# Optimization experiments

Measured on AMD Instinct MI355X. Metric: run time of the kernel, lower is better.

The kernel has to match this reference:

```python
import jax, jax.numpy as jnp
import numpy as np

N = 10000          # nodes
E = 320000         # edges (~32 neighbors/node)
HID = 128          # hidden_channels
NF = 128           # num_filters
NG = 50            # num_gaussians
NB = 6             # num_interactions
CUT = 10.0         # cutoff


def ssp(x):
    # ShiftedSoftplus: softplus(x) - log(2)
    return jax.nn.softplus(x) - jnp.log(2.0).astype(x.dtype)


def setup_inputs() -> dict:
    key = jax.random.key(0)
    ks = jax.random.split(key, 16)
    z = jax.random.randint(ks[0], (N,), 0, 100)
    pos = jax.random.uniform(ks[1], (N, 3), dtype=jnp.float32) * 5.0  # box so d < cutoff
    row = jax.random.randint(ks[2], (E,), 0, N)
    off = jax.random.randint(ks[3], (E,), 1, N)  # avoid self-loops (radius_graph excludes them)
    col = (row + off) % N
    edge_index = jnp.stack([row, col], axis=0)
    nrm = lambda k, s: 0.1 * jax.random.normal(k, s, dtype=jnp.float32)
    return {
        "z": z,
        "pos": pos,
        "edge_index": edge_index,
        "emb": nrm(ks[4], (100, HID)),
        "mlp_w1": nrm(ks[5], (NB, NG, NF)),
        "mlp_b1": jnp.zeros((NB, NF), jnp.float32),
        "mlp_w2": nrm(ks[6], (NB, NF, NF)),
        "mlp_b2": jnp.zeros((NB, NF), jnp.float32),
        "cl1_w": nrm(ks[7], (NB, HID, NF)),
        "cl2_w": nrm(ks[8], (NB, NF, HID)),
        "cl2_b": jnp.zeros((NB, HID), jnp.float32),
        "lin_w": nrm(ks[9], (NB, HID, HID)),
        "lin_b": jnp.zeros((NB, HID), jnp.float32),
        "out_w1": nrm(ks[10], (HID, HID // 2)),
        "out_b1": jnp.zeros((HID // 2,), jnp.float32),
        "out_w2": nrm(ks[11], (HID // 2, 1)),
        "out_b2": jnp.zeros((1,), jnp.float32),
    }


def schnet_fwd(z, pos, edge_index, emb, mlp_w1, mlp_b1, mlp_w2, mlp_b2,
               cl1_w, cl2_w, cl2_b, lin_w, lin_b, out_w1, out_b1, out_w2, out_b2):
    row, col = edge_index[0], edge_index[1]  # j (source), i (target)
    d = jnp.linalg.norm(pos[row] - pos[col], axis=-1)  # [E]
    offsets = jnp.linspace(0.0, CUT, NG)
    coeff = -0.5 / (offsets[1] - offsets[0]) ** 2
    edge_attr = jnp.exp(coeff * (d[:, None] - offsets) ** 2)  # [E, NG]
    C = 0.5 * (jnp.cos(d * jnp.pi / CUT) + 1.0)  # cosine cutoff [E]
    h = emb[z]  # [N, HID]
    n = h.shape[0]
    for k in range(NB):
        # per-edge filter MLP
        W = ssp(edge_attr @ mlp_w1[k] + mlp_b1[k]) @ mlp_w2[k] + mlp_b2[k]
        W = W * C[:, None]  # [E, NF]
        x = h @ cl1_w[k]  # lin1 (no bias) [N, NF]
        msg = x[row] * W  # gather + modulate
        agg = jax.ops.segment_sum(msg, col, num_segments=n)  # scatter-add to targets
        x = agg @ cl2_w[k] + cl2_b[k]  # lin2 [N, HID]
        x = ssp(x)
        x = x @ lin_w[k] + lin_b[k]  # InteractionBlock.lin
        h = h + x  # residual
    h = ssp(h @ out_w1 + out_b1)
    return h @ out_w2 + out_b2  # [N, 1]


def reference(z, pos, edge_index, emb, mlp_w1, mlp_b1, mlp_w2, mlp_b2,
              cl1_w, cl2_w, cl2_b, lin_w, lin_b, out_w1, out_b1, out_w2, out_b2):
    return schnet_fwd(z, pos, edge_index, emb, mlp_w1, mlp_b1, mlp_w2, mlp_b2,
                      cl1_w, cl2_w, cl2_b, lin_w, lin_b, out_w1, out_b1, out_w2, out_b2)
```

## Files before the change

kernel.cpp:

```cpp
#include <hip/hip_runtime.h>
#include <math.h>

#define N_NODES 10000
#define N_EDGES 320000
#define HID 128
#define NF 128
#define NG 50
#define NB 6
#define SCAN_CH 40
#define WFRAG_PER_K 24576
#define NWF_PER_MAT 32768
#define TBL_M 2048
#define DMAX 8.6602540378f

typedef __attribute__((ext_vector_type(8))) short bf16x8;
typedef __attribute__((ext_vector_type(4))) float f32x4;
typedef __attribute__((ext_vector_type(4))) unsigned int u32x4;

__device__ __forceinline__ int pi_map(int f) {
  return (f & ~31) | ((f & 15) << 1) | ((f >> 4) & 1);
}
__device__ __forceinline__ int pinv_map(int g) {
  return (g & ~31) | ((g & 1) << 4) | ((g & 31) >> 1);
}

__device__ __forceinline__ unsigned short f2bf(float f) {
  unsigned u = __float_as_uint(f);
  u += 0x7FFFu + ((u >> 16) & 1u);
  return (unsigned short)(u >> 16);
}
__device__ __forceinline__ float bf2f(unsigned short s) {
  return __uint_as_float(((unsigned)s) << 16);
}
__device__ __forceinline__ unsigned pack2f(float a, float b) {
  return ((__float_as_uint(a) + 0x8000u) >> 16) |
         ((__float_as_uint(b) + 0x8000u) & 0xFFFF0000u);
}
__device__ __forceinline__ float ssp_fast(float x) {
  float t = __expf(-fabsf(x));
  return fmaxf(x, 0.0f) + __logf(1.0f + t) - 0.69314718055994530942f;
}

__global__ __launch_bounds__(256) void k_embed(const int* __restrict__ z,
                                               const float* __restrict__ emb,
                                               float* __restrict__ h) {
  int t = blockIdx.x * 256 + threadIdx.x;
  if (t >= N_NODES * HID) return;
  int i = t >> 7, c = t & 127;
  h[t] = emb[z[i] * HID + c];
}

__global__ __launch_bounds__(256) void k_hist(const int* __restrict__ col,
                                              int* __restrict__ count) {
  int e = blockIdx.x * 256 + threadIdx.x;
  if (e < N_EDGES) atomicAdd(&count[col[e]], 1);
}

__global__ __launch_bounds__(256) void k_scan(const int* __restrict__ count,
                                              int* __restrict__ rowptr,
                                              int* __restrict__ cursor) {
  __shared__ int s_part[256];
  int t = threadIdx.x;
  int begin = t * SCAN_CH, end = min(begin + SCAN_CH, N_NODES);
  int s = 0;
  for (int i = begin; i < end; i++) s += count[i];
  s_part[t] = s;
  __syncthreads();
  for (int off = 1; off < 256; off <<= 1) {
    int v = (t >= off) ? s_part[t - off] : 0;
    __syncthreads();
    s_part[t] += v;
    __syncthreads();
  }
  int run = (t > 0) ? s_part[t - 1] : 0;
  for (int i = begin; i < end; i++) {
    rowptr[i] = run;
    cursor[i] = run;
    run += count[i];
  }
  if (t == 255) rowptr[N_NODES] = N_EDGES;
}

__global__ __launch_bounds__(256) void k_scatter(const int* __restrict__ row,
                                                 const int* __restrict__ col,
                                                 const float* __restrict__ pos,
                                                 int* __restrict__ cursor,
                                                 int2* __restrict__ sorted_ru) {
  int e = blockIdx.x * 256 + threadIdx.x;
  if (e >= N_EDGES) return;
  int c = col[e], r = row[e];
  float dx = pos[3 * r + 0] - pos[3 * c + 0];
  float dy = pos[3 * r + 1] - pos[3 * c + 1];
  float dz = pos[3 * r + 2] - pos[3 * c + 2];
  float d = sqrtf(dx * dx + dy * dy + dz * dz);
  int p = atomicAdd(&cursor[c], 1);
  float u = d * ((float)(TBL_M - 1) / DMAX);
  sorted_ru[p] = make_int2(r, __float_as_int(u));
}

__global__ __launch_bounds__(256) void k_pack(const float* __restrict__ w1,
                                              const float* __restrict__ w2,
                                              unsigned short* __restrict__ wf) {
  const float* w1k = w1 + (size_t)blockIdx.x * NG * NF;
  const float* w2k = w2 + (size_t)blockIdx.x * NF * NF;
  unsigned short* wfk = wf + (size_t)blockIdx.x * WFRAG_PER_K;
  for (int inst = threadIdx.x; inst < 3072; inst += 256) {
    int fi = inst >> 8;
    int wv = (inst >> 6) & 3;
    int lane = inst & 63;
    int r16 = lane & 15, kgrp = lane >> 4;
    bf16x8 v;
#pragma unroll
    for (int j = 0; j < 8; ++j) {
      float val;
      if (fi < 4) {
        int ncol = wv * 32 + r16 + (fi >> 1) * 16;
        int k = (fi & 1) * 32 + kgrp * 8 + j;
        val = (k < NG) ? w1k[k * NF + ncol] : 0.f;
      } else {
        int fi2 = fi - 4;
        int ncol = wv * 32 + r16 + (fi2 >> 2) * 16;
        int kpi = (fi2 & 3) * 32 + kgrp * 8 + j;
        val = w2k[pinv_map(kpi) * NF + ncol];
      }
      v[j] = (short)f2bf(val);
    }
    *(bf16x8*)&wfk[inst * 8] = v;
  }
}

__global__ __launch_bounds__(256) void k_packn(const float* __restrict__ cl1,
                                               const float* __restrict__ cl2,
                                               const float* __restrict__ lin,
                                               unsigned short* __restrict__ nwf) {
  const int mat = blockIdx.x;
  const float* src = (mat < 6) ? cl1 + (size_t)mat * HID * NF
                   : (mat < 12) ? cl2 + (size_t)(mat - 6) * NF * HID
                                : lin + (size_t)(mat - 12) * HID * HID;
  unsigned short* dst = nwf + (size_t)mat * NWF_PER_MAT;
  for (int inst = threadIdx.x; inst < 2048; inst += 256) {
    int fi = inst >> 8;
    int wv = (inst >> 6) & 3;
    int lane = inst & 63;
    int r16 = lane & 15, kgrp = lane >> 4;
    int ncol = wv * 32 + r16 + (fi >> 2) * 16;
    int kb = fi & 3;
    bf16x8 fh, fl;
#pragma unroll
    for (int j = 0; j < 8; ++j) {
      float val = src[(kb * 32 + kgrp * 8 + j) * 128 + ncol];
      unsigned short hh = f2bf(val);
      fh[j] = (short)hh;
      fl[j] = (short)f2bf(val - bf2f(hh));
    }
    *(bf16x8*)&dst[((fi * 4 + wv) * 64 + lane) * 8] = fh;
    *(bf16x8*)&dst[(((fi + 8) * 4 + wv) * 64 + lane) * 8] = fl;
  }
}

__device__ __forceinline__ void stage_hilo(unsigned short* s_hi, unsigned short* s_lo,
                                           int rr, int c4, float4 v) {
  int cs = c4 ^ ((rr & 7) << 3);
  unsigned hax = (__float_as_uint(v.x) + 0x8000u) & 0xFFFF0000u;
  unsigned hay = (__float_as_uint(v.y) + 0x8000u) & 0xFFFF0000u;
  unsigned haz = (__float_as_uint(v.z) + 0x8000u) & 0xFFFF0000u;
  unsigned haw = (__float_as_uint(v.w) + 0x8000u) & 0xFFFF0000u;
  float lx = v.x - __uint_as_float(hax);
  float ly = v.y - __uint_as_float(hay);
  float lz = v.z - __uint_as_float(haz);
  float lw = v.w - __uint_as_float(haw);
  *(uint2*)&s_hi[rr * 128 + cs] = make_uint2((hax >> 16) | hay, (haz >> 16) | haw);
  *(uint2*)&s_lo[rr * 128 + cs] = make_uint2(pack2f(lx, ly), pack2f(lz, lw));
}

__device__ __forceinline__ int swz_idx(int row, int col) {
  return row * 128 + (((col & ~7) ^ ((row & 7) << 3)) | (col & 7));
}

#define KSTEP(accA, accB, kb, BH_A, BL_A, BH_B, BL_B, rowoff)                  \
  {                                                                            \
    bf16x8 ahi = *(const bf16x8*)&s_hi[(rowoff) + (((kb) * 32 + kb0) ^ swz)];  \
    bf16x8 alo = *(const bf16x8*)&s_lo[(rowoff) + (((kb) * 32 + kb0) ^ swz)];  \
    accA = __builtin_amdgcn_mfma_f32_16x16x32_bf16(ahi, BH_A, accA, 0, 0, 0);  \
    accA = __builtin_amdgcn_mfma_f32_16x16x32_bf16(alo, BH_A, accA, 0, 0, 0);  \
    accA = __builtin_amdgcn_mfma_f32_16x16x32_bf16(ahi, BL_A, accA, 0, 0, 0);  \
    accB = __builtin_amdgcn_mfma_f32_16x16x32_bf16(ahi, BH_B, accB, 0, 0, 0);  \
    accB = __builtin_amdgcn_mfma_f32_16x16x32_bf16(alo, BH_B, accB, 0, 0, 0);  \
    accB = __builtin_amdgcn_mfma_f32_16x16x32_bf16(ahi, BL_B, accB, 0, 0, 0);  \
  }
#define MFMA_ALL()                                          \
  {                                                         \
    const int ro0 = r16 * 128;                              \
    KSTEP(a00, a01, 0, bh00, bl00, bh10, bl10, ro0);        \
    KSTEP(a00, a01, 1, bh01, bl01, bh11, bl11, ro0);        \
    KSTEP(a00, a01, 2, bh02, bl02, bh12, bl12, ro0);        \
    KSTEP(a00, a01, 3, bh03, bl03, bh13, bl13, ro0);        \
    const int ro1 = (16 + r16) * 128;                       \
    KSTEP(a10, a11, 0, bh00, bl00, bh10, bl10, ro1);        \
    KSTEP(a10, a11, 1, bh01, bl01, bh11, bl11, ro1);        \
    KSTEP(a10, a11, 2, bh02, bl02, bh12, bl12, ro1);        \
    KSTEP(a10, a11, 3, bh03, bl03, bh13, bl13, ro1);        \
  }
#define LOAD_FRAGS(wfp)                                                              \
  const bf16x8* np = (const bf16x8*)(wfp);                                           \
  const bf16x8 bh00 = np[(0 * 4 + wvid) * 64 + lane], bh01 = np[(1 * 4 + wvid) * 64 + lane], \
               bh02 = np[(2 * 4 + wvid) * 64 + lane], bh03 = np[(3 * 4 + wvid) * 64 + lane], \
               bh10 = np[(4 * 4 + wvid) * 64 + lane], bh11 = np[(5 * 4 + wvid) * 64 + lane], \
               bh12 = np[(6 * 4 + wvid) * 64 + lane], bh13 = np[(7 * 4 + wvid) * 64 + lane], \
               bl00 = np[(8 * 4 + wvid) * 64 + lane], bl01 = np[(9 * 4 + wvid) * 64 + lane], \
               bl02 = np[(10 * 4 + wvid) * 64 + lane], bl03 = np[(11 * 4 + wvid) * 64 + lane], \
               bl10 = np[(12 * 4 + wvid) * 64 + lane], bl11 = np[(13 * 4 + wvid) * 64 + lane], \
               bl12 = np[(14 * 4 + wvid) * 64 + lane], bl13 = np[(15 * 4 + wvid) * 64 + lane];

__global__ __launch_bounds__(256) void k_ngemm(const float* __restrict__ in,
                                               const unsigned short* __restrict__ wf,
                                               float* __restrict__ out,
                                               int nrows) {
  __shared__ __align__(16) float s_buf[32 * 128];
  unsigned short* s_hi = (unsigned short*)s_buf;
  unsigned short* s_lo = s_hi + 32 * 128;
  float* s_out = s_buf;

  const int tid = threadIdx.x;
  const int lane = tid & 63;
  const int wvid = tid >> 6;
  const int r16 = lane & 15;
  const int kgrp = lane >> 4;
  const int kb0 = kgrp * 8;
  const int nc0 = wvid * 32 + r16;
  const int nc1 = nc0 + 16;
  const int r0 = blockIdx.x * 32;

#pragma unroll
  for (int j = 0; j < 4; ++j) {
    int idx4 = j * 256 + tid;
    int rr = idx4 >> 5;
    int c4 = (idx4 & 31) << 2;
    float4 v = make_float4(0.f, 0.f, 0.f, 0.f);
    if (r0 + rr < nrows) v = *(const float4*)&in[(size_t)(r0 + rr) * 128 + c4];
    stage_hilo(s_hi, s_lo, rr, c4, v);
  }
  LOAD_FRAGS(wf);
  __syncthreads();

  f32x4 a00 = {0.f, 0.f, 0.f, 0.f}, a01 = a00, a10 = a00, a11 = a00;
  const int swz = (r16 & 7) << 3;
  MFMA_ALL();
  __syncthreads();

#pragma unroll
  for (int r = 0; r < 4; ++r) {
    int er0 = kgrp * 4 + r, er1 = 16 + kgrp * 4 + r;
    s_out[er0 * 128 + (nc0 ^ ((er0 & 7) << 2))] = a00[r];
    s_out[er0 * 128 + (nc1 ^ ((er0 & 7) << 2))] = a01[r];
    s_out[er1 * 128 + (nc0 ^ ((er1 & 7) << 2))] = a10[r];
    s_out[er1 * 128 + (nc1 ^ ((er1 & 7) << 2))] = a11[r];
  }
  __syncthreads();

#pragma unroll
  for (int j = 0; j < 4; ++j) {
    int idx4 = j * 256 + tid;
    int rr = idx4 >> 5;
    int c4 = (idx4 & 31) << 2;
    if (r0 + rr >= nrows) continue;
    int cs = c4 ^ ((rr & 7) << 2);
    *(float4*)&out[(size_t)(r0 + rr) * 128 + c4] = *(float4*)&s_out[rr * 128 + cs];
  }
}

__global__ __launch_bounds__(256) void k_ngemm2(const float* __restrict__ agg,
                                                const unsigned short* __restrict__ wf_cl2,
                                                const float* __restrict__ b_cl2,
                                                const unsigned short* __restrict__ wf_lin,
                                                const float* __restrict__ b_lin,
                                                float* __restrict__ h,
                                                int nrows) {
  __shared__ __align__(16) float s_buf[32 * 128];
  unsigned short* s_hi = (unsigned short*)s_buf;
  unsigned short* s_lo = s_hi + 32 * 128;
  float* s_out = s_buf;

  const int tid = threadIdx.x;
  const int lane = tid & 63;
  const int wvid = tid >> 6;
  const int r16 = lane & 15;
  const int kgrp = lane >> 4;
  const int kb0 = kgrp * 8;
  const int nc0 = wvid * 32 + r16;
  const int nc1 = nc0 + 16;
  const int r0 = blockIdx.x * 32;
  const int swz = (r16 & 7) << 3;

#pragma unroll
  for (int j = 0; j < 4; ++j) {
    int idx4 = j * 256 + tid;
    int rr = idx4 >> 5;
    int c4 = (idx4 & 31) << 2;
    float4 v = make_float4(0.f, 0.f, 0.f, 0.f);
    if (r0 + rr < nrows) v = *(const float4*)&agg[(size_t)(r0 + rr) * 128 + c4];
    stage_hilo(s_hi, s_lo, rr, c4, v);
  }
  const float bc0 = b_cl2[nc0], bc1 = b_cl2[nc1];
  const float bl0_ = b_lin[nc0], bl1_ = b_lin[nc1];
  __syncthreads();

  f32x4 a00 = {0.f, 0.f, 0.f, 0.f}, a01 = a00, a10 = a00, a11 = a00;
  {
    LOAD_FRAGS(wf_cl2);
    MFMA_ALL();
  }
  __syncthreads();

#pragma unroll
  for (int r = 0; r < 4; ++r) {
    int er0 = kgrp * 4 + r, er1 = 16 + kgrp * 4 + r;
    float t00 = ssp_fast(a00[r] + bc0);
    float t01 = ssp_fast(a01[r] + bc1);
    float t10 = ssp_fast(a10[r] + bc0);
    float t11 = ssp_fast(a11[r] + bc1);
    unsigned u;
    u = (__float_as_uint(t00) + 0x8000u) & 0xFFFF0000u;
    s_hi[swz_idx(er0, nc0)] = (unsigned short)(u >> 16);
    s_lo[swz_idx(er0, nc0)] = (unsigned short)(pack2f(t00 - __uint_as_float(u), 0.f));
    u = (__float_as_uint(t01) + 0x8000u) & 0xFFFF0000u;
    s_hi[swz_idx(er0, nc1)] = (unsigned short)(u >> 16);
    s_lo[swz_idx(er0, nc1)] = (unsigned short)(pack2f(t01 - __uint_as_float(u), 0.f));
    u = (__float_as_uint(t10) + 0x8000u) & 0xFFFF0000u;
    s_hi[swz_idx(er1, nc0)] = (unsigned short)(u >> 16);
    s_lo[swz_idx(er1, nc0)] = (unsigned short)(pack2f(t10 - __uint_as_float(u), 0.f));
    u = (__float_as_uint(t11) + 0x8000u) & 0xFFFF0000u;
    s_hi[swz_idx(er1, nc1)] = (unsigned short)(u >> 16);
    s_lo[swz_idx(er1, nc1)] = (unsigned short)(pack2f(t11 - __uint_as_float(u), 0.f));
  }
  __syncthreads();

  f32x4 c00 = {0.f, 0.f, 0.f, 0.f}, c01 = c00, c10 = c00, c11 = c00;
  {
    LOAD_FRAGS(wf_lin);
    const int ro0 = r16 * 128;
    KSTEP(c00, c01, 0, bh00, bl00, bh10, bl10, ro0);
    KSTEP(c00, c01, 1, bh01, bl01, bh11, bl11, ro0);
    KSTEP(c00, c01, 2, bh02, bl02, bh12, bl12, ro0);
    KSTEP(c00, c01, 3, bh03, bl03, bh13, bl13, ro0);
    const int ro1 = (16 + r16) * 128;
    KSTEP(c10, c11, 0, bh00, bl00, bh10, bl10, ro1);
    KSTEP(c10, c11, 1, bh01, bl01, bh11, bl11, ro1);
    KSTEP(c10, c11, 2, bh02, bl02, bh12, bl12, ro1);
    KSTEP(c10, c11, 3, bh03, bl03, bh13, bl13, ro1);
  }
  __syncthreads();

#pragma unroll
  for (int r = 0; r < 4; ++r) {
    int er0 = kgrp * 4 + r, er1 = 16 + kgrp * 4 + r;
    s_out[er0 * 128 + (nc0 ^ ((er0 & 7) << 2))] = c00[r] + bl0_;
    s_out[er0 * 128 + (nc1 ^ ((er0 & 7) << 2))] = c01[r] + bl1_;
    s_out[er1 * 128 + (nc0 ^ ((er1 & 7) << 2))] = c10[r] + bl0_;
    s_out[er1 * 128 + (nc1 ^ ((er1 & 7) << 2))] = c11[r] + bl1_;
  }
  __syncthreads();

#pragma unroll
  for (int j = 0; j < 4; ++j) {
    int idx4 = j * 256 + tid;
    int rr = idx4 >> 5;
    int c4 = (idx4 & 31) << 2;
    if (r0 + rr >= nrows) continue;
    int cs = c4 ^ ((rr & 7) << 2);
    float4 v = *(float4*)&s_out[rr * 128 + cs];
    float* dst = &h[(size_t)(r0 + rr) * 128 + c4];
    float4 o = *(const float4*)dst;
    v.x += o.x; v.y += o.y; v.z += o.z; v.w += o.w;
    *(float4*)dst = v;
  }
}

__global__ __launch_bounds__(256) void k_ngemm3(const float* __restrict__ agg,
                                                const unsigned short* __restrict__ wf_cl2,
                                                const float* __restrict__ b_cl2,
                                                const unsigned short* __restrict__ wf_lin,
                                                const float* __restrict__ b_lin,
                                                const unsigned short* __restrict__ wf_cl1n,
                                                float* __restrict__ h,
                                                float* __restrict__ x,
                                                int nrows) {
  __shared__ __align__(16) float s_buf[32 * 128];
  unsigned short* s_hi = (unsigned short*)s_buf;
  unsigned short* s_lo = s_hi + 32 * 128;
  float* s_out = s_buf;

  const int tid = threadIdx.x;
  const int lane = tid & 63;
  const int wvid = tid >> 6;
  const int r16 = lane & 15;
  const int kgrp = lane >> 4;
  const int kb0 = kgrp * 8;
  const int nc0 = wvid * 32 + r16;
  const int nc1 = nc0 + 16;
  const int r0 = blockIdx.x * 32;
  const int swz = (r16 & 7) << 3;

#pragma unroll
  for (int j = 0; j < 4; ++j) {
    int idx4 = j * 256 + tid;
    int rr = idx4 >> 5;
    int c4 = (idx4 & 31) << 2;
    float4 v = make_float4(0.f, 0.f, 0.f, 0.f);
    if (r0 + rr < nrows) v = *(const float4*)&agg[(size_t)(r0 + rr) * 128 + c4];
    stage_hilo(s_hi, s_lo, rr, c4, v);
  }
  const float bc0 = b_cl2[nc0], bc1 = b_cl2[nc1];
  const float bl0_ = b_lin[nc0], bl1_ = b_lin[nc1];
  __syncthreads();

  f32x4 a00 = {0.f, 0.f, 0.f, 0.f}, a01 = a00, a10 = a00, a11 = a00;
  {
    LOAD_FRAGS(wf_cl2);
    MFMA_ALL();
  }
  __syncthreads();

#pragma unroll
  for (int r = 0; r < 4; ++r) {
    int er0 = kgrp * 4 + r, er1 = 16 + kgrp * 4 + r;
    float t00 = ssp_fast(a00[r] + bc0);
    float t01 = ssp_fast(a01[r] + bc1);
    float t10 = ssp_fast(a10[r] + bc0);
    float t11 = ssp_fast(a11[r] + bc1);
    unsigned u;
    u = (__float_as_uint(t00) + 0x8000u) & 0xFFFF0000u;
    s_hi[swz_idx(er0, nc0)] = (unsigned short)(u >> 16);
    s_lo[swz_idx(er0, nc0)] = (unsigned short)(pack2f(t00 - __uint_as_float(u), 0.f));
    u = (__float_as_uint(t01) + 0x8000u) & 0xFFFF0000u;
    s_hi[swz_idx(er0, nc1)] = (unsigned short)(u >> 16);
    s_lo[swz_idx(er0, nc1)] = (unsigned short)(pack2f(t01 - __uint_as_float(u), 0.f));
    u = (__float_as_uint(t10) + 0x8000u) & 0xFFFF0000u;
    s_hi[swz_idx(er1, nc0)] = (unsigned short)(u >> 16);
    s_lo[swz_idx(er1, nc0)] = (unsigned short)(pack2f(t10 - __uint_as_float(u), 0.f));
    u = (__float_as_uint(t11) + 0x8000u) & 0xFFFF0000u;
    s_hi[swz_idx(er1, nc1)] = (unsigned short)(u >> 16);
    s_lo[swz_idx(er1, nc1)] = (unsigned short)(pack2f(t11 - __uint_as_float(u), 0.f));
  }
  __syncthreads();

  f32x4 c00 = {0.f, 0.f, 0.f, 0.f}, c01 = c00, c10 = c00, c11 = c00;
  {
    LOAD_FRAGS(wf_lin);
    const int ro0 = r16 * 128;
    KSTEP(c00, c01, 0, bh00, bl00, bh10, bl10, ro0);
    KSTEP(c00, c01, 1, bh01, bl01, bh11, bl11, ro0);
    KSTEP(c00, c01, 2, bh02, bl02, bh12, bl12, ro0);
    KSTEP(c00, c01, 3, bh03, bl03, bh13, bl13, ro0);
    const int ro1 = (16 + r16) * 128;
    KSTEP(c10, c11, 0, bh00, bl00, bh10, bl10, ro1);
    KSTEP(c10, c11, 1, bh01, bl01, bh11, bl11, ro1);
    KSTEP(c10, c11, 2, bh02, bl02, bh12, bl12, ro1);
    KSTEP(c10, c11, 3, bh03, bl03, bh13, bl13, ro1);
  }
  __syncthreads();

#pragma unroll
  for (int r = 0; r < 4; ++r) {
    int er0 = kgrp * 4 + r, er1 = 16 + kgrp * 4 + r;
    s_out[er0 * 128 + (nc0 ^ ((er0 & 7) << 2))] = c00[r] + bl0_;
    s_out[er0 * 128 + (nc1 ^ ((er0 & 7) << 2))] = c01[r] + bl1_;
    s_out[er1 * 128 + (nc0 ^ ((er1 & 7) << 2))] = c10[r] + bl0_;
    s_out[er1 * 128 + (nc1 ^ ((er1 & 7) << 2))] = c11[r] + bl1_;
  }
  __syncthreads();

  float4 vv[4];
#pragma unroll
  for (int j = 0; j < 4; ++j) {
    int idx4 = j * 256 + tid;
    int rr = idx4 >> 5;
    int c4 = (idx4 & 31) << 2;
    int cs = c4 ^ ((rr & 7) << 2);
    float4 v = *(float4*)&s_out[rr * 128 + cs];
    if (r0 + rr < nrows) {
      float4 o = *(const float4*)&h[(size_t)(r0 + rr) * 128 + c4];
      v.x += o.x; v.y += o.y; v.z += o.z; v.w += o.w;
    } else {
      v = make_float4(0.f, 0.f, 0.f, 0.f);
    }
    vv[j] = v;
  }
  __syncthreads();
#pragma unroll
  for (int j = 0; j < 4; ++j) {
    int idx4 = j * 256 + tid;
    int rr = idx4 >> 5;
    int c4 = (idx4 & 31) << 2;
    stage_hilo(s_hi, s_lo, rr, c4, vv[j]);
    if (r0 + rr < nrows) *(float4*)&h[(size_t)(r0 + rr) * 128 + c4] = vv[j];
  }
  __syncthreads();

  a00 = (f32x4){0.f, 0.f, 0.f, 0.f}; a01 = a00; a10 = a00; a11 = a00;
  {
    LOAD_FRAGS(wf_cl1n);
    MFMA_ALL();
  }
  __syncthreads();

#pragma unroll
  for (int r = 0; r < 4; ++r) {
    int er0 = kgrp * 4 + r, er1 = 16 + kgrp * 4 + r;
    s_out[er0 * 128 + (nc0 ^ ((er0 & 7) << 2))] = a00[r];
    s_out[er0 * 128 + (nc1 ^ ((er0 & 7) << 2))] = a01[r];
    s_out[er1 * 128 + (nc0 ^ ((er1 & 7) << 2))] = a10[r];
    s_out[er1 * 128 + (nc1 ^ ((er1 & 7) << 2))] = a11[r];
  }
  __syncthreads();

#pragma unroll
  for (int j = 0; j < 4; ++j) {
    int idx4 = j * 256 + tid;
    int rr = idx4 >> 5;
    int c4 = (idx4 & 31) << 2;
    if (r0 + rr >= nrows) continue;
    int cs = c4 ^ ((rr & 7) << 2);
    *(float4*)&x[(size_t)(r0 + rr) * 128 + c4] = *(float4*)&s_out[rr * 128 + cs];
  }
}

__global__ __launch_bounds__(256) void k_tbuild(
    const unsigned short* __restrict__ wf_all, const float* __restrict__ b1_all,
    const float* __restrict__ b2_all, float* __restrict__ T_all) {
  __shared__ __align__(16) unsigned short s_rbf[128 * 64];
  __shared__ __align__(16) unsigned short s_t1[128 * 128];
  __shared__ float s_C[128];

  const int kk = blockIdx.x >> 4;
  const int sb = blockIdx.x & 15;
  const int s0 = sb * 128;
  const unsigned short* wf = wf_all + (size_t)kk * WFRAG_PER_K;
  const float* b1 = b1_all + (size_t)kk * NF;
  const float* b2 = b2_all + (size_t)kk * NF;
  float* T = T_all + (size_t)kk * TBL_M * NF;

  const int tid = threadIdx.x;
  const int lane = tid & 63;
  const int wvid = tid >> 6;
  const int r16 = lane & 15;
  const int kgrp = lane >> 4;
  const int kb0 = kgrp * 8;
  const int nc0 = wvid * 32 + r16;
  const int nc1 = nc0 + 16;
  const int pcol = wvid * 32 + 2 * r16;

  const bf16x8* wp = (const bf16x8*)wf;
#define FR(fi) wp[((fi) * 4 + wvid) * 64 + lane]
  const bf16x8 w1_00 = FR(0), w1_10 = FR(1), w1_01 = FR(2), w1_11 = FR(3);
  const bf16x8 w2_00 = FR(4), w2_10 = FR(5), w2_20 = FR(6), w2_30 = FR(7);
  const bf16x8 w2_01 = FR(8), w2_11 = FR(9), w2_21 = FR(10), w2_31 = FR(11);
#undef FR
  const float b1n0 = b1[nc0], b1n1 = b1[nc1];
  const float b2n0 = b2[nc0], b2n1 = b2[nc1];

  {
    const int e = tid >> 1, gh = tid & 1;
    const float d = (float)(s0 + e) * (DMAX / (float)(TBL_M - 1));
    if (gh == 0) s_C[e] = 0.5f * (__cosf(d * 0.31415926535897932f) + 1.0f);
    const float step = 10.0f / 49.0f;
    const float coeff = -0.5f / (step * step);
    const int swz = (e & 7) << 3;
#pragma unroll
    for (int o = 0; o < 4; ++o) {
      int g0 = gh * 32 + o * 8;
      float vv[8];
#pragma unroll
      for (int j = 0; j < 8; ++j) {
        int g = g0 + j;
        float t = d - step * (float)g;
        vv[j] = (g < NG) ? __expf(coeff * t * t) : 0.0f;
      }
      u32x4 pk;
      pk[0] = pack2f(vv[0], vv[1]);
      pk[1] = pack2f(vv[2], vv[3]);
      pk[2] = pack2f(vv[4], vv[5]);
      pk[3] = pack2f(vv[6], vv[7]);
      *(u32x4*)&s_rbf[e * 64 + (g0 ^ swz)] = pk;
    }
  }
  __syncthreads();

  {
    const int swz = (r16 & 7) << 3;
    for (int mt = 0; mt < 8; ++mt) {
      const unsigned short* rp = &s_rbf[(mt * 16 + r16) * 64];
      bf16x8 a0 = *(const bf16x8*)&rp[(0 + kb0) ^ swz];
      bf16x8 a1 = *(const bf16x8*)&rp[(32 + kb0) ^ swz];
      f32x4 ac0 = {0.f, 0.f, 0.f, 0.f};
      f32x4 ac1 = {0.f, 0.f, 0.f, 0.f};
      ac0 = __builtin_amdgcn_mfma_f32_16x16x32_bf16(a0, w1_00, ac0, 0, 0, 0);
      ac0 = __builtin_amdgcn_mfma_f32_16x16x32_bf16(a1, w1_10, ac0, 0, 0, 0);
      ac1 = __builtin_amdgcn_mfma_f32_16x16x32_bf16(a0, w1_01, ac1, 0, 0, 0);
      ac1 = __builtin_amdgcn_mfma_f32_16x16x32_bf16(a1, w1_11, ac1, 0, 0, 0);
#pragma unroll
      for (int r = 0; r < 4; ++r) {
        int er = mt * 16 + kgrp * 4 + r;
        float v0 = ssp_fast(ac0[r] + b1n0);
        float v1 = ssp_fast(ac1[r] + b1n1);
        *(unsigned*)&s_t1[er * 128 + (pcol ^ ((er & 7) << 3))] = pack2f(v0, v1);
      }
    }
  }
  __syncthreads();

  {
    const int swz = (r16 & 7) << 3;
    for (int mt = 0; mt < 8; ++mt) {
      const unsigned short* tp = &s_t1[(mt * 16 + r16) * 128];
      bf16x8 a0 = *(const bf16x8*)&tp[(0 + kb0) ^ swz];
      bf16x8 a1 = *(const bf16x8*)&tp[(32 + kb0) ^ swz];
      bf16x8 a2 = *(const bf16x8*)&tp[(64 + kb0) ^ swz];
      bf16x8 a3 = *(const bf16x8*)&tp[(96 + kb0) ^ swz];
      f32x4 ac0 = {0.f, 0.f, 0.f, 0.f};
      f32x4 ac1 = {0.f, 0.f, 0.f, 0.f};
      ac0 = __builtin_amdgcn_mfma_f32_16x16x32_bf16(a0, w2_00, ac0, 0, 0, 0);
      ac0 = __builtin_amdgcn_mfma_f32_16x16x32_bf16(a1, w2_10, ac0, 0, 0, 0);
      ac0 = __builtin_amdgcn_mfma_f32_16x16x32_bf16(a2, w2_20, ac0, 0, 0, 0);
      ac0 = __builtin_amdgcn_mfma_f32_16x16x32_bf16(a3, w2_30, ac0, 0, 0, 0);
      ac1 = __builtin_amdgcn_mfma_f32_16x16x32_bf16(a0, w2_01, ac1, 0, 0, 0);
      ac1 = __builtin_amdgcn_mfma_f32_16x16x32_bf16(a1, w2_11, ac1, 0, 0, 0);
      ac1 = __builtin_amdgcn_mfma_f32_16x16x32_bf16(a2, w2_21, ac1, 0, 0, 0);
      ac1 = __builtin_amdgcn_mfma_f32_16x16x32_bf16(a3, w2_31, ac1, 0, 0, 0);
#pragma unroll
      for (int r = 0; r < 4; ++r) {
        int er = mt * 16 + kgrp * 4 + r;
        float Cc = s_C[er];
        float2 v = make_float2((ac0[r] + b2n0) * Cc, (ac1[r] + b2n1) * Cc);
        *(float2*)&T[(size_t)(s0 + er) * NF + pcol] = v;
      }
    }
  }
}

__global__ __launch_bounds__(256) void k_tpack(const float* __restrict__ T_all,
                                               unsigned* __restrict__ Tp_all) {
  size_t t = (size_t)blockIdx.x * 256 + threadIdx.x;
  int f = (int)(t & 127);
  size_t rem = t >> 7;
  int i = (int)(rem & (TBL_M - 1));
  int kk = (int)(rem >> 11);
  const float* T = T_all + (size_t)kk * TBL_M * NF;
  int pf = pi_map(f);
  float lo = T[(size_t)i * NF + pf];
  float hi = T[(size_t)min(i + 1, TBL_M - 1) * NF + pf];
  Tp_all[t] = pack2f(lo, hi);
}

__global__ __launch_bounds__(256) void k_aggr(const int2* __restrict__ ru,
                                              const int* __restrict__ rowptr,
                                              const unsigned* __restrict__ Tp,
                                              const float* __restrict__ x,
                                              float* __restrict__ agg) {
  __shared__ float s_part[128];
  const int n = blockIdx.x;
  const int half = threadIdx.x >> 7;
  const int f = threadIdx.x & 127;
  const int beg = rowptr[n], end = rowptr[n + 1];
  const int mid = beg + ((end - beg + 1) >> 1);
  int e = half ? mid : beg;
  const int stop = half ? end : mid;

  float a[8] = {0.f, 0.f, 0.f, 0.f, 0.f, 0.f, 0.f, 0.f};
  for (; e + 8 <= stop; e += 8) {
    int2 p[8];
#pragma unroll
    for (int q = 0; q < 8; ++q) p[q] = ru[e + q];
    unsigned tv[8];
    float fr[8];
#pragma unroll
    for (int q = 0; q < 8; ++q) {
      float u = __int_as_float(p[q].y);
      int i0 = min((int)u, TBL_M - 2);
      fr[q] = u - (float)i0;
      tv[q] = Tp[(size_t)i0 * NF + f];
    }
    float xv[8];
#pragma unroll
    for (int q = 0; q < 8; ++q) xv[q] = x[(size_t)p[q].x * NF + f];
#pragma unroll
    for (int q = 0; q < 8; ++q) {
      float lo = __uint_as_float(tv[q] << 16);
      float hi = __uint_as_float(tv[q] & 0xFFFF0000u);
      a[q] = fmaf(fmaf(fr[q], hi - lo, lo), xv[q], a[q]);
    }
  }
  for (; e + 4 <= stop; e += 4) {
    int2 p[4];
#pragma unroll
    for (int q = 0; q < 4; ++q) p[q] = ru[e + q];
#pragma unroll
    for (int q = 0; q < 4; ++q) {
      float u = __int_as_float(p[q].y);
      int i0 = min((int)u, TBL_M - 2);
      float frq = u - (float)i0;
      unsigned tvq = Tp[(size_t)i0 * NF + f];
      float lo = __uint_as_float(tvq << 16);
      float hi = __uint_as_float(tvq & 0xFFFF0000u);
      a[q] = fmaf(fmaf(frq, hi - lo, lo), x[(size_t)p[q].x * NF + f], a[q]);
    }
  }
  for (; e < stop; ++e) {
    int2 p = ru[e];
    float u = __int_as_float(p.y);
    int i0 = min((int)u, TBL_M - 2);
    float frq = u - (float)i0;
    unsigned tvq = Tp[(size_t)i0 * NF + f];
    float lo = __uint_as_float(tvq << 16);
    float hi = __uint_as_float(tvq & 0xFFFF0000u);
    a[0] = fmaf(fmaf(frq, hi - lo, lo), x[(size_t)p.x * NF + f], a[0]);
  }
  float part = ((a[0] + a[1]) + (a[2] + a[3])) + ((a[4] + a[5]) + (a[6] + a[7]));
  if (half) s_part[f] = part;
  __syncthreads();
  if (!half) agg[(size_t)n * NF + f] = part + s_part[f];
}

__global__ __launch_bounds__(256) void k_out(const float* __restrict__ h,
                                             const float* __restrict__ w1,
                                             const float* __restrict__ b1,
                                             const float* __restrict__ w2,
                                             const float* __restrict__ b2,
                                             float* __restrict__ out) {
  int wid = threadIdx.x >> 6;
  int lane = threadIdx.x & 63;
  int i = blockIdx.x * 4 + wid;
  if (i >= N_NODES) return;
  const float* __restrict__ hr = h + i * HID;
  float acc = b1[lane];
#pragma unroll 8
  for (int k = 0; k < HID; k++) acc = fmaf(hr[k], w1[k * 64 + lane], acc);
  float p = ssp_fast(acc) * w2[lane];
#pragma unroll
  for (int off = 32; off; off >>= 1) p += __shfl_down(p, off);
  if (lane == 0) out[i] = p + b2[0];
}

extern "C" void kernel_launch(void* const* d_in, const int* in_sizes, int n_in,
                              void* d_out, int out_size, void* d_ws, size_t ws_size,
                              hipStream_t stream) {
  const int* z = (const int*)d_in[0];
  const float* pos = (const float*)d_in[1];
  const int* eidx = (const int*)d_in[2];
  const float* emb = (const float*)d_in[3];
  const float* mlp_w1 = (const float*)d_in[4];
  const float* mlp_b1 = (const float*)d_in[5];
  const float* mlp_w2 = (const float*)d_in[6];
  const float* mlp_b2 = (const float*)d_in[7];
  const float* cl1_w = (const float*)d_in[8];
  const float* cl2_w = (const float*)d_in[9];
  const float* cl2_b = (const float*)d_in[10];
  const float* lin_w = (const float*)d_in[11];
  const float* lin_b = (const float*)d_in[12];
  const float* out_w1 = (const float*)d_in[13];
  const float* out_b1 = (const float*)d_in[14];
  const float* out_w2 = (const float*)d_in[15];
  const float* out_b2 = (const float*)d_in[16];
  float* out = (float*)d_out;

  float* h = (float*)d_ws;
  float* x = h + N_NODES * HID;
  float* agg = x + N_NODES * HID;
  int* count = (int*)(agg + N_NODES * HID);
  int* rowptr = count + 10240;
  int* cursor = rowptr + 10240;
  int2* sorted_ru = (int2*)(cursor + 10240);
  unsigned short* wfrag = (unsigned short*)(sorted_ru + N_EDGES);
  unsigned short* nwf = wfrag + (size_t)NB * WFRAG_PER_K;
  float* Tbl = (float*)(nwf + (size_t)18 * NWF_PER_MAT);
  unsigned* Tp = (unsigned*)(Tbl + (size_t)NB * TBL_M * NF);
  const int* row = eidx;
  const int* col = eidx + N_EDGES;

  hipMemsetAsync(count, 0, 10240 * sizeof(int), stream);
  k_hist<<<(N_EDGES + 255) / 256, 256, 0, stream>>>(col, count);
  k_scan<<<1, 256, 0, stream>>>(count, rowptr, cursor);
  k_scatter<<<(N_EDGES + 255) / 256, 256, 0, stream>>>(row, col, pos, cursor,
                                                       sorted_ru);

  k_pack<<<NB, 256, 0, stream>>>(mlp_w1, mlp_w2, wfrag);
  k_packn<<<18, 256, 0, stream>>>(cl1_w, cl2_w, lin_w, nwf);
  k_tbuild<<<NB * 16, 256, 0, stream>>>(wfrag, mlp_b1, mlp_b2, Tbl);
  k_tpack<<<(NB * TBL_M * NF) / 256, 256, 0, stream>>>(Tbl, Tp);

  k_embed<<<(N_NODES * HID + 255) / 256, 256, 0, stream>>>(z, emb, h);

  const int NGB = (N_NODES + 31) / 32;
  k_ngemm<<<NGB, 256, 0, stream>>>(h, nwf + (size_t)0 * NWF_PER_MAT, x, N_NODES);
  for (int k = 0; k < NB; k++) {
    k_aggr<<<N_NODES, 256, 0, stream>>>(sorted_ru, rowptr,
                                        Tp + (size_t)k * TBL_M * NF, x, agg);
    if (k < NB - 1) {
      k_ngemm3<<<NGB, 256, 0, stream>>>(
          agg, nwf + (size_t)(6 + k) * NWF_PER_MAT, cl2_b + (size_t)k * HID,
          nwf + (size_t)(12 + k) * NWF_PER_MAT, lin_b + (size_t)k * HID,
          nwf + (size_t)(k + 1) * NWF_PER_MAT, h, x, N_NODES);
    } else {
      k_ngemm2<<<NGB, 256, 0, stream>>>(
          agg, nwf + (size_t)(6 + k) * NWF_PER_MAT, cl2_b + (size_t)k * HID,
          nwf + (size_t)(12 + k) * NWF_PER_MAT, lin_b + (size_t)k * HID, h, N_NODES);
    }
  }

  k_out<<<(N_NODES + 3) / 4, 256, 0, stream>>>(h, out_w1, out_b1, out_w2, out_b2, out);
}
```

Baseline: 382.2 us.

## Split node aggregation across four wavefronts with float2 features and LDS-staged edges

Rewrites the per-node gather-aggregate kernel so each of four wavefronts handles every fourth edge, with each lane covering two features through float2/uint2 loads. Edge records are first staged cooperatively into shared memory instead of every thread loading them redundantly. Partial sums from the wavefronts are reduced through shared memory at the end. The intent is wider loads, fewer redundant index loads and more edge-level parallelism per block, at the cost of extra barriers and less per-thread unrolling, which lowers the number of independent loads in flight.

```diff
diff --git a/kernel.cpp b/kernel.cpp
--- a/kernel.cpp
+++ b/kernel.cpp
@@ -657,68 +657,70 @@
                                               const unsigned* __restrict__ Tp,
                                               const float* __restrict__ x,
                                               float* __restrict__ agg) {
-  __shared__ float s_part[128];
+  __shared__ int2 s_ru[256];
+  __shared__ float s_part[3 * 128];
+  const int tid = threadIdx.x;
+  const int wvid = tid >> 6;
+  const int lane = tid & 63;
+  const int f2 = lane * 2;
   const int n = blockIdx.x;
-  const int half = threadIdx.x >> 7;
-  const int f = threadIdx.x & 127;
   const int beg = rowptr[n], end = rowptr[n + 1];
-  const int mid = beg + ((end - beg + 1) >> 1);
-  int e = half ? mid : beg;
-  const int stop = half ? end : mid;
-
-  float a[8] = {0.f, 0.f, 0.f, 0.f, 0.f, 0.f, 0.f, 0.f};
-  for (; e + 8 <= stop; e += 8) {
-    int2 p[8];
-#pragma unroll
-    for (int q = 0; q < 8; ++q) p[q] = ru[e + q];
-    unsigned tv[8];
-    float fr[8];
-#pragma unroll
-    for (int q = 0; q < 8; ++q) {
-      float u = __int_as_float(p[q].y);
-      int i0 = min((int)u, TBL_M - 2);
-      fr[q] = u - (float)i0;
-      tv[q] = Tp[(size_t)i0 * NF + f];
-    }
-    float xv[8];
-#pragma unroll
-    for (int q = 0; q < 8; ++q) xv[q] = x[(size_t)p[q].x * NF + f];
-#pragma unroll
-    for (int q = 0; q < 8; ++q) {
-      float lo = __uint_as_float(tv[q] << 16);
-      float hi = __uint_as_float(tv[q] & 0xFFFF0000u);
-      a[q] = fmaf(fmaf(fr[q], hi - lo, lo), xv[q], a[q]);
-    }
-  }
-  for (; e + 4 <= stop; e += 4) {
-    int2 p[4];
-#pragma unroll
-    for (int q = 0; q < 4; ++q) p[q] = ru[e + q];
-#pragma unroll
-    for (int q = 0; q < 4; ++q) {
-      float u = __int_as_float(p[q].y);
-      int i0 = min((int)u, TBL_M - 2);
-      float frq = u - (float)i0;
-      unsigned tvq = Tp[(size_t)i0 * NF + f];
-      float lo = __uint_as_float(tvq << 16);
-      float hi = __uint_as_float(tvq & 0xFFFF0000u);
-      a[q] = fmaf(fmaf(frq, hi - lo, lo), x[(size_t)p[q].x * NF + f], a[q]);
-    }
-  }
-  for (; e < stop; ++e) {
-    int2 p = ru[e];
-    float u = __int_as_float(p.y);
-    int i0 = min((int)u, TBL_M - 2);
-    float frq = u - (float)i0;
-    unsigned tvq = Tp[(size_t)i0 * NF + f];
-    float lo = __uint_as_float(tvq << 16);
-    float hi = __uint_as_float(tvq & 0xFFFF0000u);
-    a[0] = fmaf(fmaf(frq, hi - lo, lo), x[(size_t)p.x * NF + f], a[0]);
-  }
-  float part = ((a[0] + a[1]) + (a[2] + a[3])) + ((a[4] + a[5]) + (a[6] + a[7]));
-  if (half) s_part[f] = part;
-  __syncthreads();
-  if (!half) agg[(size_t)n * NF + f] = part + s_part[f];
+
+  float ax0 = 0.f, ay0 = 0.f, ax1 = 0.f, ay1 = 0.f;
+  for (int cs = beg; cs < end; cs += 256) {
+    const int cnt = min(256, end - cs);
+    if (tid < cnt) s_ru[tid] = ru[cs + tid];
+    __syncthreads();
+    int j = wvid;
+    for (; j + 4 < cnt; j += 8) {
+      int2 p0 = s_ru[j];
+      int2 p1 = s_ru[j + 4];
+      float u0 = __int_as_float(p0.y), u1 = __int_as_float(p1.y);
+      int i0 = min((int)u0, TBL_M - 2), i1 = min((int)u1, TBL_M - 2);
+      float fr0 = u0 - (float)i0, fr1 = u1 - (float)i1;
+      uint2 t0 = *(const uint2*)&Tp[(size_t)i0 * NF + f2];
+      uint2 t1 = *(const uint2*)&Tp[(size_t)i1 * NF + f2];
+      float2 x0 = *(const float2*)&x[(size_t)p0.x * NF + f2];
+      float2 x1 = *(const float2*)&x[(size_t)p1.x * NF + f2];
+      float lo, hi;
+      lo = __uint_as_float(t0.x << 16); hi = __uint_as_float(t0.x & 0xFFFF0000u);
+      ax0 = fmaf(fmaf(fr0, hi - lo, lo), x0.x, ax0);
+      lo = __uint_as_float(t0.y << 16); hi = __uint_as_float(t0.y & 0xFFFF0000u);
+      ay0 = fmaf(fmaf(fr0, hi - lo, lo), x0.y, ay0);
+      lo = __uint_as_float(t1.x << 16); hi = __uint_as_float(t1.x & 0xFFFF0000u);
+      ax1 = fmaf(fmaf(fr1, hi - lo, lo), x1.x, ax1);
+      lo = __uint_as_float(t1.y << 16); hi = __uint_as_float(t1.y & 0xFFFF0000u);
+      ay1 = fmaf(fmaf(fr1, hi - lo, lo), x1.y, ay1);
+    }
+    for (; j < cnt; j += 4) {
+      int2 p0 = s_ru[j];
+      float u0 = __int_as_float(p0.y);
+      int i0 = min((int)u0, TBL_M - 2);
+      float fr0 = u0 - (float)i0;
+      uint2 t0 = *(const uint2*)&Tp[(size_t)i0 * NF + f2];
+      float2 x0 = *(const float2*)&x[(size_t)p0.x * NF + f2];
+      float lo, hi;
+      lo = __uint_as_float(t0.x << 16); hi = __uint_as_float(t0.x & 0xFFFF0000u);
+      ax0 = fmaf(fmaf(fr0, hi - lo, lo), x0.x, ax0);
+      lo = __uint_as_float(t0.y << 16); hi = __uint_as_float(t0.y & 0xFFFF0000u);
+      ay0 = fmaf(fmaf(fr0, hi - lo, lo), x0.y, ay0);
+    }
+    __syncthreads();
+  }
+
+  float fx = ax0 + ax1, fy = ay0 + ay1;
+  if (wvid > 0) {
+    *(float2*)&s_part[(wvid - 1) * 128 + f2] = make_float2(fx, fy);
+  }
+  __syncthreads();
+  if (wvid == 0) {
+#pragma unroll
+    for (int w = 0; w < 3; ++w) {
+      fx += s_part[w * 128 + f2];
+      fy += s_part[w * 128 + f2 + 1];
+    }
+    *(float2*)&agg[(size_t)n * NF + f2] = make_float2(fx, fy);
+  }
 }
 
 __global__ __launch_bounds__(256) void k_out(const float* __restrict__ h,
```

Result: faster. 360.0 us (-5.8%).
